# Optimization experiments

Measured on AMD Instinct MI355X. Metric: run time of the kernel, lower is better.

Reference implementation:

```python
import jax, jax.numpy as jnp
import numpy as np

V, E, H, B, S = 50000, 512, 1024, 256, 256


def setup_inputs() -> dict:
    key = jax.random.key(0)
    ks = jax.random.split(key, 8)
    inputs = jax.random.randint(ks[0], (B, S), 0, V)
    emb = jax.random.normal(ks[1], (V, E), dtype=jnp.float32)
    sx, sh = 1.0 / np.sqrt(E), 1.0 / np.sqrt(H)  # ~orthogonal column scale
    Wx_f = jax.random.normal(ks[2], (E, 4 * H), dtype=jnp.float32) * sx
    Wh_f = jax.random.normal(ks[3], (H, 4 * H), dtype=jnp.float32) * sh
    Wx_b = jax.random.normal(ks[4], (E, 4 * H), dtype=jnp.float32) * sx
    Wh_b = jax.random.normal(ks[5], (H, 4 * H), dtype=jnp.float32) * sh
    # gate order i, f, o, c ; forget-gate bias initialized to 1 as in the source
    bias = jnp.concatenate([jnp.zeros(H), jnp.ones(H), jnp.zeros(H), jnp.zeros(H)]).astype(jnp.float32)
    W_hq = jax.random.normal(ks[6], (H, 10), dtype=jnp.float32) * sh
    b_q = jnp.zeros(10, dtype=jnp.float32)
    return {"inputs": inputs, "emb": emb, "Wx_f": Wx_f, "Wh_f": Wh_f, "b_f": bias,
            "Wx_b": Wx_b, "Wh_b": Wh_b, "b_b": bias, "W_hq": W_hq, "b_q": b_q}


def _lstm_final_h(x_tbe, Wx, Wh, b):
    """x_tbe: [S,B,E] time-major. Returns final hidden state [B,H]."""
    h0 = jnp.zeros((x_tbe.shape[1], H), dtype=x_tbe.dtype)
    c0 = jnp.zeros_like(h0)

    def cell(carry, X):
        h, c = carry
        g = X @ Wx + h @ Wh + b          # [B, 4H] fused gate pre-activations
        i, f, o, ct = jnp.split(g, 4, axis=-1)
        c = jax.nn.sigmoid(f) * c + jax.nn.sigmoid(i) * jnp.tanh(ct)
        h = jax.nn.sigmoid(o) * jnp.tanh(c)
        return (h, c), None

    (h, _), _ = jax.lax.scan(cell, (h0, c0), x_tbe)
    return h


def reference(inputs, emb, Wx_f, Wh_f, b_f, Wx_b, Wh_b, b_b, W_hq, b_q):
    x = emb[inputs]                      # [B,S,E]
    x = jnp.transpose(x, (1, 0, 2))      # [S,B,E] time-major
    h_fwd = _lstm_final_h(x, Wx_f, Wh_f, b_f)
    h_bwd = _lstm_final_h(x[::-1], Wx_b, Wh_b, b_b)
    logits = (h_fwd + h_bwd) @ W_hq + b_q
    return jax.nn.softmax(logits, axis=1)
```

## Files before the change

kernel.cpp:

```cpp
#include <hip/hip_runtime.h>

#define S_LEN 256
#define BATCH 256
#define EDIM 512
#define HDIM 1024
#define LDS_BYTES 131072

typedef short short8 __attribute__((ext_vector_type(8)));
typedef float f32x4 __attribute__((ext_vector_type(4)));
typedef unsigned long long u64;
typedef unsigned short us;

__device__ __forceinline__ us f2bf(float f) {
  unsigned u = __float_as_uint(f);
  u = u + 0x7FFFu + ((u >> 16) & 1u);
  return (us)(u >> 16);
}
__device__ __forceinline__ float bf2f(us s) {
  return __uint_as_float(((unsigned)s) << 16);
}
__device__ __forceinline__ float sigf(float x) { return 1.0f / (1.0f + __expf(-x)); }
__device__ __forceinline__ float tanh_(float x) { return 2.0f / (1.0f + __expf(-2.0f * x)) - 1.0f; }

#define MFMA(d, a, b) d = __builtin_amdgcn_mfma_f32_16x16x32_bf16(a, b, d, 0, 0, 0)

__device__ __forceinline__ short8 load_hfrag(const us* p) {
  union { u64 d[2]; short8 v; } u;
  u.d[0] = __hip_atomic_load((const u64*)p,       __ATOMIC_RELAXED, __HIP_MEMORY_SCOPE_AGENT);
  u.d[1] = __hip_atomic_load((const u64*)(p + 4), __ATOMIC_RELAXED, __HIP_MEMORY_SCOPE_AGENT);
  return u.v;
}
__device__ __forceinline__ short8 ldf(const us* p) {
  union { uint4 d; short8 v; } u;
  u.d = *(const uint4*)p;
  return u.v;
}


__global__ void gather_embed(const int* __restrict__ inputs, const float* __restrict__ emb,
                             us* __restrict__ Xf) {
  int T = blockIdx.x * 256 + threadIdx.x;
  int kt = T & 15;
  int b  = (T >> 4) & 255;
  int s  = T >> 12;
  int vid = inputs[b * S_LEN + s];
  const float* src = emb + (size_t)vid * EDIM + kt * 32;
  int c = b & 15;
  us* ub = Xf + ((size_t)(s * 16 + kt) * 16 + (b >> 4)) * 512;
#pragma unroll
  for (int q = 0; q < 4; ++q) {
    float4 v0 = *(const float4*)(src + q * 8);
    float4 v1 = *(const float4*)(src + q * 8 + 4);
    us o[8] = { f2bf(v0.x), f2bf(v0.y), f2bf(v0.z), f2bf(v0.w),
                f2bf(v1.x), f2bf(v1.y), f2bf(v1.z), f2bf(v1.w) };
    *(uint4*)(ub + (size_t)(c + 16 * q) * 8) = *(const uint4*)o;
  }
}

__global__ void pack_w(const float* __restrict__ Wx_f, const float* __restrict__ Wh_f,
                       const float* __restrict__ Wx_b, const float* __restrict__ Wh_b,
                       us* __restrict__ Wxp, us* __restrict__ Whp) {
  int T = blockIdx.x * 256 + threadIdx.x;
  int c = T & 15;
  int q = (T >> 4) & 3;
  int t = (T >> 6) & 7;
  int r = T >> 9;
  int kit = r % 48;
  int jbd = r / 48;
  int jb  = jbd & 31;
  int dir = jbd >> 5;
  int g = t >> 1, h16 = t & 1;
  int n = g * 1024 + jb * 32 + h16 * 16 + c;
  const float* W; int k0;
  if (kit < 16) { W = dir ? Wx_b : Wx_f; k0 = kit * 32 + q * 8; }
  else          { W = dir ? Wh_b : Wh_f; k0 = (kit - 16) * 32 + q * 8; }
  us o[8];
#pragma unroll
  for (int e = 0; e < 8; ++e) o[e] = f2bf(W[(size_t)(k0 + e) * 4096 + n]);
  us* dst;
  if (kit < 16) dst = Wxp + (((size_t)(dir * 32 + jb) * 16 + kit) * 8 + t) * 512;
  else          dst = Whp + (((size_t)(dir * 32 + jb) * 32 + (kit - 16)) * 8 + t) * 512;
  *(uint4*)(dst + (size_t)(c + 16 * q) * 8) = *(const uint4*)o;
}

__global__ __launch_bounds__(256, 1) void lstm_main(
    const us* __restrict__ Xf,
    const us* __restrict__ Wxp,
    const us* __restrict__ Whp,
    const float* __restrict__ bias_f,
    const float* __restrict__ bias_b,
    us* __restrict__ Hf,
    unsigned int* __restrict__ slots)
{
  extern __shared__ __align__(16) unsigned char smem[];

  const int bx   = blockIdx.x;
  const int xcd  = bx & 7;
  const int dir  = xcd >> 2;
  const int joct = xcd & 3;
  const int rr   = bx >> 3;
  const int jb   = joct * 8 + (rr & 7);
  const int mq   = rr >> 3;

  const int tid  = threadIdx.x;
  const int wave = tid >> 6;
  const int lane = tid & 63;
  const int mw   = wave & 1;
  const int nw   = wave >> 1;
  const int c    = lane & 15;
  const int q    = lane >> 4;
  const int lofs = lane * 8;

  {
    const uint4* src = (const uint4*)(Whp + (((size_t)(dir * 32 + jb) * 32 + 16) * 8) * 512);
    for (int i = tid; i < 8192; i += 256) *(uint4*)(smem + (size_t)i * 16) = src[i];
  }
  const float* bias = dir ? bias_b : bias_f;
  const int j = jb * 32 + nw * 16 + c;
  float bg[4];
#pragma unroll
  for (int g = 0; g < 4; ++g) bg[g] = bias[g * HDIM + j];
  __syncthreads();

  unsigned int* grp_slots = slots + (dir * 4 + mq) * (32 * 16);
  unsigned int* my_slot   = grp_slots + jb * 16;

  const int bt0 = mq * 4 + mw * 2;
  const us* xu_base  = Xf + (size_t)bt0 * 512 + lofs;
  const us* wxu = Wxp + (((size_t)(dir * 32 + jb) * 16) * 8 + nw) * 512 + lofs;
  const us* whu = Whp + (((size_t)(dir * 32 + jb) * 32) * 8 + nw) * 512 + lofs;
  const int ldsofs = (nw * 512 + lane * 8) * 2;

  float c_reg[2][4] = {{0.f,0.f,0.f,0.f},{0.f,0.f,0.f,0.f}};

  for (int s = 0; s < S_LEN; ++s) {
    const int sx = dir ? (S_LEN - 1 - s) : s;
    const int p  = s & 1;

    f32x4 acc[2][4];
#pragma unroll
    for (int mt = 0; mt < 2; ++mt)
#pragma unroll
      for (int g = 0; g < 4; ++g)
        acc[mt][g] = (f32x4){bg[g], bg[g], bg[g], bg[g]};

    {
      const us* xu = xu_base + (size_t)sx * (16 * 16 * 512);
#pragma unroll 4
      for (int k = 0; k < 16; ++k) {
        short8 a0 = ldf(xu + (size_t)k * 8192);
        short8 a1 = ldf(xu + (size_t)k * 8192 + 512);
        const us* wb = wxu + (size_t)k * 4096;
        short8 b0 = ldf(wb);
        short8 b1 = ldf(wb + 1024);
        short8 b2 = ldf(wb + 2048);
        short8 b3 = ldf(wb + 3072);
        MFMA(acc[0][0], a0, b0); MFMA(acc[0][1], a0, b1);
        MFMA(acc[0][2], a0, b2); MFMA(acc[0][3], a0, b3);
        MFMA(acc[1][0], a1, b0); MFMA(acc[1][1], a1, b1);
        MFMA(acc[1][2], a1, b2); MFMA(acc[1][3], a1, b3);
      }
    }

    if (s > 0) {
      if (tid < 32) {
        const unsigned int* sl = grp_slots + tid * 16;
        for (;;) {
          unsigned v = __hip_atomic_load(sl, __ATOMIC_RELAXED, __HIP_MEMORY_SCOPE_AGENT);
          if (!__any(v < (unsigned)s)) break;
          __builtin_amdgcn_s_sleep(1);
        }
      }
      __syncthreads();
      asm volatile("" ::: "memory");
    }

    {
      const us* hu = Hf + (((size_t)(p * 2 + dir) * 32) * 16 + bt0) * 512 + lofs;
      short8 pa0[4], pa1[4];
#pragma unroll
      for (int i = 0; i < 4; ++i) {
        pa0[i] = load_hfrag(hu + (size_t)i * 8192);
        pa1[i] = load_hfrag(hu + (size_t)i * 8192 + 512);
      }
#pragma unroll 4
      for (int k = 0; k < 16; ++k) {
        short8 a0 = pa0[k & 3], a1 = pa1[k & 3];
        pa0[k & 3] = load_hfrag(hu + (size_t)(k + 4) * 8192);
        pa1[k & 3] = load_hfrag(hu + (size_t)(k + 4) * 8192 + 512);
        const us* wb = whu + (size_t)k * 4096;
        short8 b0 = ldf(wb);
        short8 b1 = ldf(wb + 1024);
        short8 b2 = ldf(wb + 2048);
        short8 b3 = ldf(wb + 3072);
        MFMA(acc[0][0], a0, b0); MFMA(acc[0][1], a0, b1);
        MFMA(acc[0][2], a0, b2); MFMA(acc[0][3], a0, b3);
        MFMA(acc[1][0], a1, b0); MFMA(acc[1][1], a1, b1);
        MFMA(acc[1][2], a1, b2); MFMA(acc[1][3], a1, b3);
      }
#pragma unroll 4
      for (int k = 16; k < 28; ++k) {
        short8 a0 = pa0[k & 3], a1 = pa1[k & 3];
        pa0[k & 3] = load_hfrag(hu + (size_t)(k + 4) * 8192);
        pa1[k & 3] = load_hfrag(hu + (size_t)(k + 4) * 8192 + 512);
        const unsigned char* lb = smem + (size_t)(k - 16) * 8192 + ldsofs;
        short8 b0 = *(const short8*)(lb);
        short8 b1 = *(const short8*)(lb + 2048);
        short8 b2 = *(const short8*)(lb + 4096);
        short8 b3 = *(const short8*)(lb + 6144);
        MFMA(acc[0][0], a0, b0); MFMA(acc[0][1], a0, b1);
        MFMA(acc[0][2], a0, b2); MFMA(acc[0][3], a0, b3);
        MFMA(acc[1][0], a1, b0); MFMA(acc[1][1], a1, b1);
        MFMA(acc[1][2], a1, b2); MFMA(acc[1][3], a1, b3);
      }
#pragma unroll
      for (int k = 28; k < 32; ++k) {
        short8 a0 = pa0[k & 3], a1 = pa1[k & 3];
        const unsigned char* lb = smem + (size_t)(k - 16) * 8192 + ldsofs;
        short8 b0 = *(const short8*)(lb);
        short8 b1 = *(const short8*)(lb + 2048);
        short8 b2 = *(const short8*)(lb + 4096);
        short8 b3 = *(const short8*)(lb + 6144);
        MFMA(acc[0][0], a0, b0); MFMA(acc[0][1], a0, b1);
        MFMA(acc[0][2], a0, b2); MFMA(acc[0][3], a0, b3);
        MFMA(acc[1][0], a1, b0); MFMA(acc[1][1], a1, b1);
        MFMA(acc[1][2], a1, b2); MFMA(acc[1][3], a1, b3);
      }
    }

    {
      const int q2 = nw * 2 + (c >> 3);
      const int e2 = c & 7;
      const size_t ob = ((size_t)(((p ^ 1) * 2 + dir) * 32 + jb) * 16 + bt0) * 512;
#pragma unroll
      for (int mt = 0; mt < 2; ++mt) {
        us* hd = Hf + ob + (size_t)mt * 512 + (size_t)(16 * q2) * 8 + e2;
#pragma unroll
        for (int rg = 0; rg < 4; ++rg) {
          float gi = acc[mt][0][rg], gf = acc[mt][1][rg];
          float go = acc[mt][2][rg], gc = acc[mt][3][rg];
          float cn = sigf(gf) * c_reg[mt][rg] + sigf(gi) * tanh_(gc);
          c_reg[mt][rg] = cn;
          __hip_atomic_store(hd + (size_t)(q * 4 + rg) * 8, f2bf(sigf(go) * tanh_(cn)),
                             __ATOMIC_RELAXED, __HIP_MEMORY_SCOPE_AGENT);
        }
      }
    }
    asm volatile("s_waitcnt vmcnt(0)" ::: "memory");
    __syncthreads();
    if (tid == 0)
      __hip_atomic_store(my_slot, (unsigned)(s + 1), __ATOMIC_RELAXED, __HIP_MEMORY_SCOPE_AGENT);
  }
}

__global__ void final_softmax(const us* __restrict__ Hf,
                              const float* __restrict__ Whq,
                              const float* __restrict__ bq,
                              float* __restrict__ out) {
  __shared__ float red[4][10];
  const int b = blockIdx.x;
  const int tid = threadIdx.x;
  float acc[10];
#pragma unroll
  for (int qq = 0; qq < 10; ++qq) acc[qq] = 0.f;
#pragma unroll
  for (int u = 0; u < 4; ++u) {
    int j = tid * 4 + u;
    int kt = j >> 5, q2 = (j & 31) >> 3, e = j & 7;
    size_t idx = (((size_t)kt * 16 + (b >> 4)) * 512) + ((size_t)((b & 15) + 16 * q2)) * 8 + e;
    float xv = bf2f(Hf[idx]) + bf2f(Hf[(size_t)32 * 16 * 512 + idx]);
#pragma unroll
    for (int qq = 0; qq < 10; ++qq) acc[qq] += xv * Whq[j * 10 + qq];
  }
#pragma unroll
  for (int qq = 0; qq < 10; ++qq)
#pragma unroll
    for (int off = 32; off; off >>= 1) acc[qq] += __shfl_down(acc[qq], off, 64);
  if ((tid & 63) == 0)
#pragma unroll
    for (int qq = 0; qq < 10; ++qq) red[tid >> 6][qq] = acc[qq];
  __syncthreads();
  if (tid == 0) {
    float t[10];
#pragma unroll
    for (int qq = 0; qq < 10; ++qq)
      t[qq] = red[0][qq] + red[1][qq] + red[2][qq] + red[3][qq] + bq[qq];
    float mx = t[0];
#pragma unroll
    for (int qq = 1; qq < 10; ++qq) mx = fmaxf(mx, t[qq]);
    float sum = 0.f;
#pragma unroll
    for (int qq = 0; qq < 10; ++qq) { t[qq] = __expf(t[qq] - mx); sum += t[qq]; }
    float inv = 1.0f / sum;
#pragma unroll
    for (int qq = 0; qq < 10; ++qq) out[b * 10 + qq] = t[qq] * inv;
  }
}

extern "C" void kernel_launch(void* const* d_in, const int* in_sizes, int n_in,
                              void* d_out, int out_size, void* d_ws, size_t ws_size,
                              hipStream_t stream) {
  const int*   inputs = (const int*)d_in[0];
  const float* emb    = (const float*)d_in[1];
  const float* Wx_f   = (const float*)d_in[2];
  const float* Wh_f   = (const float*)d_in[3];
  const float* b_f    = (const float*)d_in[4];
  const float* Wx_b   = (const float*)d_in[5];
  const float* Wh_b   = (const float*)d_in[6];
  const float* b_b    = (const float*)d_in[7];
  const float* W_hq   = (const float*)d_in[8];
  const float* b_q    = (const float*)d_in[9];
  float* out = (float*)d_out;

  char* ws = (char*)d_ws;
  us* Xf  = (us*)ws;
  us* Wxp = (us*)(ws + (64ull << 20));
  us* Whp = (us*)(ws + (72ull << 20));
  us* Hf  = (us*)(ws + (88ull << 20));
  unsigned int* slt = (unsigned int*)(ws + (90ull << 20));

  hipMemsetAsync(Hf, 0, (size_t)2 * 2 * 32 * 16 * 512 * sizeof(us), stream);
  hipMemsetAsync(slt, 0, 8 * 32 * 16 * sizeof(unsigned int), stream);

  gather_embed<<<4096, 256, 0, stream>>>(inputs, emb, Xf);
  pack_w<<<6144, 256, 0, stream>>>(Wx_f, Wh_f, Wx_b, Wh_b, Wxp, Whp);

  hipFuncSetAttribute((const void*)lstm_main,
                      hipFuncAttributeMaxDynamicSharedMemorySize, LDS_BYTES);

  const us* xf_p = Xf;
  const us* wxp_p = Wxp;
  const us* whp_p = Whp;
  const float* bf_p = b_f;
  const float* bb_p = b_b;
  us* hf_p = Hf;
  unsigned int* slt_p = slt;
  void* kargs[] = { (void*)&xf_p, (void*)&wxp_p, (void*)&whp_p, (void*)&bf_p,
                    (void*)&bb_p, (void*)&hf_p, (void*)&slt_p };
  hipLaunchCooperativeKernel((void*)lstm_main, dim3(256), dim3(256), kargs, LDS_BYTES, stream);

  final_softmax<<<256, 256, 0, stream>>>(Hf, W_hq, b_q, out);
}
```

Before: 4.565 ms.

## Split LSTM step K-dimension across two wave groups with LDS reduction

Doubles the block to 512 threads and splits the per-step reduction dimension between two wave groups. Group 0 covers the first half of the x and h inputs using global Wh, and group 1 covers the second half using the LDS-resident Wh. Partial gate accumulators from group 1 are reduced into group 0 through an extra 16KB LDS buffer, and only group 0 applies the bias and computes the cell update. The aim is to halve the serial MFMA and load chain per timestep and add latency hiding, at the cost of extra barriers per step and higher register pressure from the deeper h prefetch.

```diff
diff --git a/kernel.cpp b/kernel.cpp
--- a/kernel.cpp
+++ b/kernel.cpp
@@ -4,7 +4,7 @@
 #define BATCH 256
 #define EDIM 512
 #define HDIM 1024
-#define LDS_BYTES 131072
+#define LDS_BYTES 147456
 
 typedef short short8 __attribute__((ext_vector_type(8)));
 typedef float f32x4 __attribute__((ext_vector_type(4)));
@@ -83,7 +83,7 @@
   *(uint4*)(dst + (size_t)(c + 16 * q) * 8) = *(const uint4*)o;
 }
 
-__global__ __launch_bounds__(256, 1) void lstm_main(
+__global__ __launch_bounds__(512, 1) void lstm_main(
     const us* __restrict__ Xf,
     const us* __restrict__ Wxp,
     const us* __restrict__ Whp,
@@ -104,32 +104,35 @@
 
   const int tid  = threadIdx.x;
   const int wave = tid >> 6;
+  const int kg   = wave >> 2;
+  const int wl   = wave & 3;
   const int lane = tid & 63;
-  const int mw   = wave & 1;
-  const int nw   = wave >> 1;
+  const int mw   = wl & 1;
+  const int nw   = wl >> 1;
   const int c    = lane & 15;
   const int q    = lane >> 4;
   const int lofs = lane * 8;
 
   {
     const uint4* src = (const uint4*)(Whp + (((size_t)(dir * 32 + jb) * 32 + 16) * 8) * 512);
-    for (int i = tid; i < 8192; i += 256) *(uint4*)(smem + (size_t)i * 16) = src[i];
+    for (int i = tid; i < 8192; i += 512) *(uint4*)(smem + (size_t)i * 16) = src[i];
   }
   const float* bias = dir ? bias_b : bias_f;
   const int j = jb * 32 + nw * 16 + c;
   float bg[4];
 #pragma unroll
-  for (int g = 0; g < 4; ++g) bg[g] = bias[g * HDIM + j];
+  for (int g = 0; g < 4; ++g) bg[g] = (kg == 0) ? bias[g * HDIM + j] : 0.f;
   __syncthreads();
 
   unsigned int* grp_slots = slots + (dir * 4 + mq) * (32 * 16);
   unsigned int* my_slot   = grp_slots + jb * 16;
 
   const int bt0 = mq * 4 + mw * 2;
-  const us* xu_base  = Xf + (size_t)bt0 * 512 + lofs;
+  const us* xu_base = Xf + (size_t)bt0 * 512 + lofs;
   const us* wxu = Wxp + (((size_t)(dir * 32 + jb) * 16) * 8 + nw) * 512 + lofs;
   const us* whu = Whp + (((size_t)(dir * 32 + jb) * 32) * 8 + nw) * 512 + lofs;
   const int ldsofs = (nw * 512 + lane * 8) * 2;
+  f32x4* red = (f32x4*)(smem + 131072);
 
   float c_reg[2][4] = {{0.f,0.f,0.f,0.f},{0.f,0.f,0.f,0.f}};
 
@@ -145,12 +148,13 @@
         acc[mt][g] = (f32x4){bg[g], bg[g], bg[g], bg[g]};
 
     {
-      const us* xu = xu_base + (size_t)sx * (16 * 16 * 512);
-#pragma unroll 4
-      for (int k = 0; k < 16; ++k) {
+      const us* xu = xu_base + (size_t)sx * (16 * 16 * 512) + (size_t)(kg * 8) * 8192;
+      const us* wb0 = wxu + (size_t)(kg * 8) * 4096;
+#pragma unroll
+      for (int k = 0; k < 8; ++k) {
         short8 a0 = ldf(xu + (size_t)k * 8192);
         short8 a1 = ldf(xu + (size_t)k * 8192 + 512);
-        const us* wb = wxu + (size_t)k * 4096;
+        const us* wb = wb0 + (size_t)k * 4096;
         short8 b0 = ldf(wb);
         short8 b1 = ldf(wb + 1024);
         short8 b2 = ldf(wb + 2048);
@@ -176,59 +180,94 @@
     }
 
     {
-      const us* hu = Hf + (((size_t)(p * 2 + dir) * 32) * 16 + bt0) * 512 + lofs;
-      short8 pa0[4], pa1[4];
-#pragma unroll
-      for (int i = 0; i < 4; ++i) {
+      const us* hu = Hf + (((size_t)(p * 2 + dir) * 32) * 16 + bt0) * 512 + lofs
+                   + (size_t)(kg * 16) * 8192;
+      short8 pa0[8], pa1[8];
+#pragma unroll
+      for (int i = 0; i < 8; ++i) {
         pa0[i] = load_hfrag(hu + (size_t)i * 8192);
         pa1[i] = load_hfrag(hu + (size_t)i * 8192 + 512);
       }
-#pragma unroll 4
-      for (int k = 0; k < 16; ++k) {
-        short8 a0 = pa0[k & 3], a1 = pa1[k & 3];
-        pa0[k & 3] = load_hfrag(hu + (size_t)(k + 4) * 8192);
-        pa1[k & 3] = load_hfrag(hu + (size_t)(k + 4) * 8192 + 512);
-        const us* wb = whu + (size_t)k * 4096;
-        short8 b0 = ldf(wb);
-        short8 b1 = ldf(wb + 1024);
-        short8 b2 = ldf(wb + 2048);
-        short8 b3 = ldf(wb + 3072);
-        MFMA(acc[0][0], a0, b0); MFMA(acc[0][1], a0, b1);
-        MFMA(acc[0][2], a0, b2); MFMA(acc[0][3], a0, b3);
-        MFMA(acc[1][0], a1, b0); MFMA(acc[1][1], a1, b1);
-        MFMA(acc[1][2], a1, b2); MFMA(acc[1][3], a1, b3);
-      }
-#pragma unroll 4
-      for (int k = 16; k < 28; ++k) {
-        short8 a0 = pa0[k & 3], a1 = pa1[k & 3];
-        pa0[k & 3] = load_hfrag(hu + (size_t)(k + 4) * 8192);
-        pa1[k & 3] = load_hfrag(hu + (size_t)(k + 4) * 8192 + 512);
-        const unsigned char* lb = smem + (size_t)(k - 16) * 8192 + ldsofs;
-        short8 b0 = *(const short8*)(lb);
-        short8 b1 = *(const short8*)(lb + 2048);
-        short8 b2 = *(const short8*)(lb + 4096);
-        short8 b3 = *(const short8*)(lb + 6144);
-        MFMA(acc[0][0], a0, b0); MFMA(acc[0][1], a0, b1);
-        MFMA(acc[0][2], a0, b2); MFMA(acc[0][3], a0, b3);
-        MFMA(acc[1][0], a1, b0); MFMA(acc[1][1], a1, b1);
-        MFMA(acc[1][2], a1, b2); MFMA(acc[1][3], a1, b3);
-      }
-#pragma unroll
-      for (int k = 28; k < 32; ++k) {
-        short8 a0 = pa0[k & 3], a1 = pa1[k & 3];
-        const unsigned char* lb = smem + (size_t)(k - 16) * 8192 + ldsofs;
-        short8 b0 = *(const short8*)(lb);
-        short8 b1 = *(const short8*)(lb + 2048);
-        short8 b2 = *(const short8*)(lb + 4096);
-        short8 b3 = *(const short8*)(lb + 6144);
-        MFMA(acc[0][0], a0, b0); MFMA(acc[0][1], a0, b1);
-        MFMA(acc[0][2], a0, b2); MFMA(acc[0][3], a0, b3);
-        MFMA(acc[1][0], a1, b0); MFMA(acc[1][1], a1, b1);
-        MFMA(acc[1][2], a1, b2); MFMA(acc[1][3], a1, b3);
-      }
-    }
-
-    {
+      if (kg == 0) {
+#pragma unroll
+        for (int k = 0; k < 8; ++k) {
+          short8 a0 = pa0[k], a1 = pa1[k];
+          pa0[k] = load_hfrag(hu + (size_t)(k + 8) * 8192);
+          pa1[k] = load_hfrag(hu + (size_t)(k + 8) * 8192 + 512);
+          const us* wb = whu + (size_t)k * 4096;
+          short8 b0 = ldf(wb);
+          short8 b1 = ldf(wb + 1024);
+          short8 b2 = ldf(wb + 2048);
+          short8 b3 = ldf(wb + 3072);
+          MFMA(acc[0][0], a0, b0); MFMA(acc[0][1], a0, b1);
+          MFMA(acc[0][2], a0, b2); MFMA(acc[0][3], a0, b3);
+          MFMA(acc[1][0], a1, b0); MFMA(acc[1][1], a1, b1);
+          MFMA(acc[1][2], a1, b2); MFMA(acc[1][3], a1, b3);
+        }
+#pragma unroll
+        for (int k = 8; k < 16; ++k) {
+          short8 a0 = pa0[k - 8], a1 = pa1[k - 8];
+          const us* wb = whu + (size_t)k * 4096;
+          short8 b0 = ldf(wb);
+          short8 b1 = ldf(wb + 1024);
+          short8 b2 = ldf(wb + 2048);
+          short8 b3 = ldf(wb + 3072);
+          MFMA(acc[0][0], a0, b0); MFMA(acc[0][1], a0, b1);
+          MFMA(acc[0][2], a0, b2); MFMA(acc[0][3], a0, b3);
+          MFMA(acc[1][0], a1, b0); MFMA(acc[1][1], a1, b1);
+          MFMA(acc[1][2], a1, b2); MFMA(acc[1][3], a1, b3);
+        }
+      } else {
+#pragma unroll
+        for (int k = 0; k < 8; ++k) {
+          short8 a0 = pa0[k], a1 = pa1[k];
+          pa0[k] = load_hfrag(hu + (size_t)(k + 8) * 8192);
+          pa1[k] = load_hfrag(hu + (size_t)(k + 8) * 8192 + 512);
+          const unsigned char* lb = smem + (size_t)k * 8192 + ldsofs;
+          short8 b0 = *(const short8*)(lb);
+          short8 b1 = *(const short8*)(lb + 2048);
+          short8 b2 = *(const short8*)(lb + 4096);
+          short8 b3 = *(const short8*)(lb + 6144);
+          MFMA(acc[0][0], a0, b0); MFMA(acc[0][1], a0, b1);
+          MFMA(acc[0][2], a0, b2); MFMA(acc[0][3], a0, b3);
+          MFMA(acc[1][0], a1, b0); MFMA(acc[1][1], a1, b1);
+          MFMA(acc[1][2], a1, b2); MFMA(acc[1][3], a1, b3);
+        }
+#pragma unroll
+        for (int k = 8; k < 16; ++k) {
+          short8 a0 = pa0[k - 8], a1 = pa1[k - 8];
+          const unsigned char* lb = smem + (size_t)k * 8192 + ldsofs;
+          short8 b0 = *(const short8*)(lb);
+          short8 b1 = *(const short8*)(lb + 2048);
+          short8 b2 = *(const short8*)(lb + 4096);
+          short8 b3 = *(const short8*)(lb + 6144);
+          MFMA(acc[0][0], a0, b0); MFMA(acc[0][1], a0, b1);
+          MFMA(acc[0][2], a0, b2); MFMA(acc[0][3], a0, b3);
+          MFMA(acc[1][0], a1, b0); MFMA(acc[1][1], a1, b1);
+          MFMA(acc[1][2], a1, b2); MFMA(acc[1][3], a1, b3);
+        }
+      }
+    }
+
+#pragma unroll
+    for (int mt = 0; mt < 2; ++mt) {
+      __syncthreads();
+      if (kg == 1) {
+#pragma unroll
+        for (int g = 0; g < 4; ++g) red[(g * 4 + wl) * 64 + lane] = acc[mt][g];
+      }
+      __syncthreads();
+      if (kg == 0) {
+#pragma unroll
+        for (int g = 0; g < 4; ++g) {
+          f32x4 v = red[(g * 4 + wl) * 64 + lane];
+          acc[mt][g][0] += v[0]; acc[mt][g][1] += v[1];
+          acc[mt][g][2] += v[2]; acc[mt][g][3] += v[3];
+        }
+      }
+    }
+
+    if (kg == 0) {
       const int q2 = nw * 2 + (c >> 3);
       const int e2 = c & 7;
       const size_t ob = ((size_t)(((p ^ 1) * 2 + dir) * 32 + jb) * 16 + bt0) * 512;
@@ -337,7 +376,7 @@
   unsigned int* slt_p = slt;
   void* kargs[] = { (void*)&xf_p, (void*)&wxp_p, (void*)&whp_p, (void*)&bf_p,
                     (void*)&bb_p, (void*)&hf_p, (void*)&slt_p };
-  hipLaunchCooperativeKernel((void*)lstm_main, dim3(256), dim3(256), kargs, LDS_BYTES, stream);
+  hipLaunchCooperativeKernel((void*)lstm_main, dim3(256), dim3(512), kargs, LDS_BYTES, stream);
 
   final_softmax<<<256, 256, 0, stream>>>(Hf, W_hq, b_q, out);
 }
```

Result: slower. 7.902 ms (+73.1%).
